# Optimization experiments

Hardware: AMD Instinct MI355X
Metric: run time of the kernel (lower is better)

The kernel has to match this reference:

```python
import jax, jax.numpy as jnp
import numpy as np

FEAT_DIM = 48        # feature_dim init arg
C_OUT = 2 * FEAT_DIM # conv output channels -> table row width
H = W_IMG = 256      # image spatial size -> res = C_OUT*H*W / (2*FEAT_DIM) = 65536
N_PTS = 2_000_000    # query points


def setup_inputs() -> dict:
    key = jax.random.key(0)
    k1, k2, k3, k4 = jax.random.split(key, 4)
    pts = jax.random.uniform(k1, (N_PTS, 2), dtype=jnp.float32)  # coords in [0,1)
    image = jax.random.normal(k2, (1, 3, H, W_IMG), dtype=jnp.float32)
    conv_w = jax.random.normal(k3, (C_OUT, 3, 3, 3), dtype=jnp.float32) * 0.05
    conv_b = jax.random.normal(k4, (C_OUT,), dtype=jnp.float32) * 0.05
    return {"pts": pts, "image": image, "conv_w": conv_w, "conv_b": conv_b}


def reference(pts, image, conv_w, conv_b):
    # feature_extractor: Conv2d(3, 96, k=3, SAME) -> [1, 96, 256, 256]
    feat = jax.lax.conv_general_dilated(
        image, conv_w, window_strides=(1, 1), padding="SAME",
        dimension_numbers=("NCHW", "OIHW", "NCHW"))
    feat = feat + conv_b[None, :, None, None]
    fa = feat.reshape(-1, 2 * FEAT_DIM)  # [res, 96]
    res = fa.shape[0]                    # 65536

    x = pts[:, 0] * (res - 1)
    y = pts[:, 1] * (res - 1)
    hi = res - 1 - 1e-5
    x1 = jnp.floor(jnp.clip(x, 0, hi)).astype(jnp.int32)
    y1 = jnp.floor(jnp.clip(y, 0, hi)).astype(jnp.int32)
    x2 = jnp.clip(x1 + 1, 0, res - 1)
    y2 = jnp.clip(y1 + 1, 0, res - 1)

    xw1 = (x2.astype(x.dtype) - x)[:, None]
    xw2 = (x - x1.astype(x.dtype))[:, None]
    yw1 = (y2.astype(y.dtype) - y)[:, None]
    yw2 = (y - y1.astype(y.dtype))[:, None]

    fx = fa[:, :FEAT_DIM]  # x-array half of the dual array
    fy = fa[:, FEAT_DIM:]  # y-array half
    # four gathers + weighted blend -> [N, FEAT_DIM]
    return xw1 * fx[x1] + xw2 * fx[x2] + yw1 * fy[y1] + yw2 * fy[y2]
```

## Files before the change

kernel.cpp:

```cpp
#include <hip/hip_runtime.h>
#include <hip/hip_bf16.h>

#define C_OUT 96
#define FEAT_DIM 48
#define HW 256
#define NPIX 65536
#define RES 65536
#define IMG_C 3

typedef __attribute__((ext_vector_type(4))) float f32x4;
typedef __attribute__((ext_vector_type(8))) unsigned short u16x8;
typedef __attribute__((ext_vector_type(4))) unsigned short u16x4;

static __device__ __forceinline__ unsigned short f2bf(float f) {
    unsigned u = __float_as_uint(f);
    u += 0x7fffu + ((u >> 16) & 1u);
    return (unsigned short)(u >> 16);
}
static __device__ __forceinline__ float bf2f(unsigned short h) {
    return __uint_as_float(((unsigned)h) << 16);
}

__global__ __launch_bounds__(256) void conv_kernel(
    const float* __restrict__ img,
    const float* __restrict__ w,
    const float* __restrict__ b,
    unsigned short* __restrict__ FX,
    unsigned short* __restrict__ FY)
{
    __shared__ float ws[C_OUT * 27];
    __shared__ float bs[C_OUT];
    for (int i = threadIdx.x; i < C_OUT * 27; i += blockDim.x) ws[i] = w[i];
    for (int i = threadIdx.x; i < C_OUT; i += blockDim.x) bs[i] = b[i];
    __syncthreads();

    int tid = blockIdx.x * blockDim.x + threadIdx.x;
    if (tid >= (C_OUT * NPIX) / 4) return;
    int f = tid << 2;
    int c  = f >> 16;
    int p  = f & 65535;
    int h  = p >> 8;
    int wc = p & 255;

    float a0 = bs[c], a1 = a0, a2 = a0, a3 = a0;
#pragma unroll
    for (int ci = 0; ci < IMG_C; ++ci) {
        const float* ip = img + ci * NPIX;
#pragma unroll
        for (int kh = 0; kh < 3; ++kh) {
            int hh = h + kh - 1;
            if ((unsigned)hh >= 256u) continue;
            const float* row = ip + hh * HW;
            float win[6];
#pragma unroll
            for (int k = 0; k < 6; ++k) {
                int ww = wc + k - 1;
                win[k] = ((unsigned)ww < 256u) ? row[ww] : 0.0f;
            }
            const float* wk = &ws[c * 27 + ci * 9 + kh * 3];
#pragma unroll
            for (int kw = 0; kw < 3; ++kw) {
                float wt = wk[kw];
                a0 = fmaf(win[kw + 0], wt, a0);
                a1 = fmaf(win[kw + 1], wt, a1);
                a2 = fmaf(win[kw + 2], wt, a2);
                a3 = fmaf(win[kw + 3], wt, a3);
            }
        }
    }

    int r = (unsigned)f / 96u;
    int j = f - r * 96;
    u16x4 pk;
    pk.x = f2bf(a0); pk.y = f2bf(a1); pk.z = f2bf(a2); pk.w = f2bf(a3);
    unsigned short* dst = (j < FEAT_DIM)
        ? (FX + (size_t)r * FEAT_DIM + j)
        : (FY + (size_t)r * FEAT_DIM + (j - FEAT_DIM));
    *(u16x4*)dst = pk;
}

__global__ __launch_bounds__(256) void interp_kernel(
    const float* __restrict__ pts,
    const unsigned short* __restrict__ FX,
    const unsigned short* __restrict__ FY,
    float* __restrict__ out,
    int npts)
{
    int t = blockIdx.x * blockDim.x + threadIdx.x;
    int pt = t / 6;
    int q  = t - pt * 6;
    if (pt >= npts) return;

    float px = pts[2 * pt];
    float py = pts[2 * pt + 1];
    float x = fminf(fmaxf(px * 65535.0f, 0.0f), 65535.0f);
    float y = fminf(fmaxf(py * 65535.0f, 0.0f), 65535.0f);

    int x1 = (int)x;
    int y1 = (int)y;
    int x2 = min(x1 + 1, RES - 1);
    int y2 = min(y1 + 1, RES - 1);

    float xw1 = (float)x2 - x;
    float xw2 = x - (float)x1;
    float yw1 = (float)y2 - y;
    float yw2 = y - (float)y1;

    const u16x8 A = *(const u16x8*)(FX + (size_t)x1 * FEAT_DIM + q * 8);
    const u16x8 B = *(const u16x8*)(FX + (size_t)x2 * FEAT_DIM + q * 8);
    const u16x8 C = *(const u16x8*)(FY + (size_t)y1 * FEAT_DIM + q * 8);
    const u16x8 D = *(const u16x8*)(FY + (size_t)y2 * FEAT_DIM + q * 8);

    float o[8];
#pragma unroll
    for (int k = 0; k < 8; ++k) {
        o[k] = xw1 * bf2f(A[k]) + xw2 * bf2f(B[k])
             + yw1 * bf2f(C[k]) + yw2 * bf2f(D[k]);
    }

    float* op = out + (size_t)pt * FEAT_DIM + q * 8;
    f32x4 v0 = {o[0], o[1], o[2], o[3]};
    f32x4 v1 = {o[4], o[5], o[6], o[7]};
    __builtin_nontemporal_store(v0, (f32x4*)op);
    __builtin_nontemporal_store(v1, (f32x4*)(op + 4));
}

extern "C" void kernel_launch(void* const* d_in, const int* in_sizes, int n_in,
                              void* d_out, int out_size, void* d_ws, size_t ws_size,
                              hipStream_t stream) {
    const float* pts    = (const float*)d_in[0];
    const float* image  = (const float*)d_in[1];
    const float* conv_w = (const float*)d_in[2];
    const float* conv_b = (const float*)d_in[3];
    float* out = (float*)d_out;

    unsigned short* FX = (unsigned short*)d_ws;
    unsigned short* FY = FX + (size_t)RES * FEAT_DIM;

    int npts = in_sizes[0] / 2;

    {
        int total = (C_OUT * NPIX) / 4;
        int blocks = (total + 255) / 256;
        conv_kernel<<<blocks, 256, 0, stream>>>(image, conv_w, conv_b, FX, FY);
    }
    {
        long long total = (long long)npts * 6;
        int blocks = (int)((total + 255) / 256);
        interp_kernel<<<blocks, 256, 0, stream>>>(pts, FX, FY, out, npts);
    }
}
```

Measured before the change: 232.2 us.

## Bucket-sort query points by coarse coordinates and remap blocks per XCD for locality

Adds a histogram, scan and scatter pass that bins the points into 256 buckets keyed on the high bits of their x and y table indices. It writes packed records (clipped coords plus original index) to a sorted workspace buffer. The interp kernel reads the sorted records, scatters outputs back by original index, and remaps block IDs so each XCD handles a contiguous range of sorted blocks. The aim is better L2 locality for the random table gathers, at the cost of extra passes over the points, atomics, and scattered output writes.

```diff
diff --git a/kernel.cpp b/kernel.cpp
--- a/kernel.cpp
+++ b/kernel.cpp
@@ -7,7 +7,10 @@
 #define NPIX 65536
 #define RES 65536
 #define IMG_C 3
-
+#define NBUCKET 256
+#define SCAT_PPT 8
+
+typedef __attribute__((ext_vector_type(2))) float f32x2;
 typedef __attribute__((ext_vector_type(4))) float f32x4;
 typedef __attribute__((ext_vector_type(8))) unsigned short u16x8;
 typedef __attribute__((ext_vector_type(4))) unsigned short u16x4;
@@ -20,13 +23,18 @@
 static __device__ __forceinline__ float bf2f(unsigned short h) {
     return __uint_as_float(((unsigned)h) << 16);
 }
+static __device__ __forceinline__ float clipcoord(float p) {
+    return fminf(fmaxf(p * 65535.0f, 0.0f), 65535.0f);
+}
+static __device__ __forceinline__ int bkey(float x, float y) {
+    int x1 = (int)x, y1 = (int)y;
+    return ((x1 >> 12) << 4) | (y1 >> 12);
+}
 
 __global__ __launch_bounds__(256) void conv_kernel(
-    const float* __restrict__ img,
-    const float* __restrict__ w,
+    const float* __restrict__ img, const float* __restrict__ w,
     const float* __restrict__ b,
-    unsigned short* __restrict__ FX,
-    unsigned short* __restrict__ FY)
+    unsigned short* __restrict__ FX, unsigned short* __restrict__ FY)
 {
     __shared__ float ws[C_OUT * 27];
     __shared__ float bs[C_OUT];
@@ -79,22 +87,103 @@
     *(u16x4*)dst = pk;
 }
 
+__global__ __launch_bounds__(256) void hist_kernel(
+    const float* __restrict__ pts, unsigned* __restrict__ hist, int npts)
+{
+    __shared__ unsigned lh[NBUCKET];
+    for (int i = threadIdx.x; i < NBUCKET; i += blockDim.x) lh[i] = 0;
+    __syncthreads();
+    int stride = gridDim.x * blockDim.x;
+    for (int i = blockIdx.x * blockDim.x + threadIdx.x; i < npts; i += stride) {
+        f32x2 p = *((const f32x2*)pts + i);
+        atomicAdd(&lh[bkey(clipcoord(p.x), clipcoord(p.y))], 1u);
+    }
+    __syncthreads();
+    for (int i = threadIdx.x; i < NBUCKET; i += blockDim.x)
+        if (lh[i]) atomicAdd(&hist[i], lh[i]);
+}
+
+__global__ __launch_bounds__(256) void scan_kernel(
+    const unsigned* __restrict__ hist, unsigned* __restrict__ cursor)
+{
+    __shared__ unsigned tmp[NBUCKET];
+    int t = threadIdx.x;
+    unsigned own = hist[t];
+    tmp[t] = own;
+    __syncthreads();
+#pragma unroll
+    for (int off = 1; off < NBUCKET; off <<= 1) {
+        unsigned v = (t >= off) ? tmp[t - off] : 0u;
+        __syncthreads();
+        tmp[t] += v;
+        __syncthreads();
+    }
+    cursor[t] = tmp[t] - own;
+}
+
+__global__ __launch_bounds__(256) void scatter_kernel(
+    const float* __restrict__ pts, unsigned* __restrict__ cursor,
+    f32x4* __restrict__ sorted, int npts)
+{
+    __shared__ unsigned lh[NBUCKET];
+    __shared__ unsigned lbase[NBUCKET];
+    int t = threadIdx.x;
+    for (int i = t; i < NBUCKET; i += blockDim.x) lh[i] = 0;
+    __syncthreads();
+
+    int start = blockIdx.x * (blockDim.x * SCAT_PPT);
+    float xs[SCAT_PPT], ys[SCAT_PPT];
+    int keys[SCAT_PPT];
+#pragma unroll
+    for (int k = 0; k < SCAT_PPT; ++k) {
+        int i = start + k * blockDim.x + t;
+        if (i < npts) {
+            f32x2 p = *((const f32x2*)pts + i);
+            xs[k] = clipcoord(p.x);
+            ys[k] = clipcoord(p.y);
+            keys[k] = bkey(xs[k], ys[k]);
+            atomicAdd(&lh[keys[k]], 1u);
+        } else keys[k] = -1;
+    }
+    __syncthreads();
+    for (int i = t; i < NBUCKET; i += blockDim.x)
+        lbase[i] = lh[i] ? atomicAdd(&cursor[i], lh[i]) : 0u;
+    __syncthreads();
+    for (int i = t; i < NBUCKET; i += blockDim.x) lh[i] = 0;
+    __syncthreads();
+#pragma unroll
+    for (int k = 0; k < SCAT_PPT; ++k) {
+        if (keys[k] >= 0) {
+            unsigned slot = lbase[keys[k]] + atomicAdd(&lh[keys[k]], 1u);
+            int i = start + k * blockDim.x + t;
+            f32x4 rec;
+            rec.x = xs[k]; rec.y = ys[k];
+            rec.z = __uint_as_float((unsigned)i); rec.w = 0.0f;
+            sorted[slot] = rec;
+        }
+    }
+}
+
 __global__ __launch_bounds__(256) void interp_kernel(
-    const float* __restrict__ pts,
+    const f32x4* __restrict__ sorted,
     const unsigned short* __restrict__ FX,
     const unsigned short* __restrict__ FY,
-    float* __restrict__ out,
-    int npts)
-{
-    int t = blockIdx.x * blockDim.x + threadIdx.x;
-    int pt = t / 6;
-    int q  = t - pt * 6;
-    if (pt >= npts) return;
-
-    float px = pts[2 * pt];
-    float py = pts[2 * pt + 1];
-    float x = fminf(fmaxf(px * 65535.0f, 0.0f), 65535.0f);
-    float y = fminf(fmaxf(py * 65535.0f, 0.0f), 65535.0f);
+    float* __restrict__ out, int npts, int nblk)
+{
+    int orig = blockIdx.x;
+    int xcd = orig & 7;
+    int q8 = nblk >> 3, r8 = nblk & 7;
+    int base = (xcd < r8) ? xcd * (q8 + 1) : r8 * (q8 + 1) + (xcd - r8) * q8;
+    int sbid = base + (orig >> 3);
+
+    int t = sbid * blockDim.x + threadIdx.x;
+    int s = t / 6;
+    int q = t - s * 6;
+    if (s >= npts) return;
+
+    f32x4 rec = sorted[s];
+    float x = rec.x, y = rec.y;
+    unsigned idx = __float_as_uint(rec.z);
 
     int x1 = (int)x;
     int y1 = (int)y;
@@ -106,10 +195,11 @@
     float yw1 = (float)y2 - y;
     float yw2 = y - (float)y1;
 
-    const u16x8 A = *(const u16x8*)(FX + (size_t)x1 * FEAT_DIM + q * 8);
-    const u16x8 B = *(const u16x8*)(FX + (size_t)x2 * FEAT_DIM + q * 8);
-    const u16x8 C = *(const u16x8*)(FY + (size_t)y1 * FEAT_DIM + q * 8);
-    const u16x8 D = *(const u16x8*)(FY + (size_t)y2 * FEAT_DIM + q * 8);
+    int qo = q * 8;
+    const u16x8 A = *(const u16x8*)(FX + (size_t)x1 * FEAT_DIM + qo);
+    const u16x8 B = *(const u16x8*)(FX + (size_t)x2 * FEAT_DIM + qo);
+    const u16x8 C = *(const u16x8*)(FY + (size_t)y1 * FEAT_DIM + qo);
+    const u16x8 D = *(const u16x8*)(FY + (size_t)y2 * FEAT_DIM + qo);
 
     float o[8];
 #pragma unroll
@@ -118,7 +208,7 @@
              + yw1 * bf2f(C[k]) + yw2 * bf2f(D[k]);
     }
 
-    float* op = out + (size_t)pt * FEAT_DIM + q * 8;
+    float* op = out + (size_t)idx * FEAT_DIM + qo;
     f32x4 v0 = {o[0], o[1], o[2], o[3]};
     f32x4 v1 = {o[4], o[5], o[6], o[7]};
     __builtin_nontemporal_store(v0, (f32x4*)op);
@@ -134,19 +224,32 @@
     const float* conv_b = (const float*)d_in[3];
     float* out = (float*)d_out;
 
-    unsigned short* FX = (unsigned short*)d_ws;
+    int npts = in_sizes[0] / 2;
+
+    char* wsb = (char*)d_ws;
+    f32x4* sorted = (f32x4*)wsb;
+    size_t sorted_bytes = ((size_t)npts * 16 + 255) & ~(size_t)255;
+    unsigned short* FX = (unsigned short*)(wsb + sorted_bytes);
     unsigned short* FY = FX + (size_t)RES * FEAT_DIM;
-
-    int npts = in_sizes[0] / 2;
+    unsigned* hist   = (unsigned*)(wsb + sorted_bytes + 2 * (size_t)RES * FEAT_DIM * 2);
+    unsigned* cursor = hist + NBUCKET;
+
+    hipMemsetAsync(hist, 0, NBUCKET * sizeof(unsigned), stream);
 
     {
         int total = (C_OUT * NPIX) / 4;
-        int blocks = (total + 255) / 256;
-        conv_kernel<<<blocks, 256, 0, stream>>>(image, conv_w, conv_b, FX, FY);
+        conv_kernel<<<(total + 255) / 256, 256, 0, stream>>>(image, conv_w, conv_b, FX, FY);
+    }
+    hist_kernel<<<1024, 256, 0, stream>>>(pts, hist, npts);
+    scan_kernel<<<1, 256, 0, stream>>>(hist, cursor);
+    {
+        int per_block = 256 * SCAT_PPT;
+        int blocks = (npts + per_block - 1) / per_block;
+        scatter_kernel<<<blocks, 256, 0, stream>>>(pts, cursor, sorted, npts);
     }
     {
         long long total = (long long)npts * 6;
-        int blocks = (int)((total + 255) / 256);
-        interp_kernel<<<blocks, 256, 0, stream>>>(pts, FX, FY, out, npts);
-    }
-}
+        int nblk = (int)((total + 255) / 256);
+        interp_kernel<<<nblk, 256, 0, stream>>>(sorted, FX, FY, out, npts, nblk);
+    }
+}
```

Result: no change. 236.2 us (+1.7%).
